# Kernel tuning notes

Measured on AMD Instinct MI355X. Metric: run time of the kernel, lower is better.

Reference implementation:

```python
import jax, jax.numpy as jnp
import numpy as np

HIDDEN = 1024
N_HEADS = 16
HEAD_DIM = HIDDEN // N_HEADS
MAX_DIST = 50
B, S = 2, 2048


def setup_inputs() -> dict:
    key = jax.random.key(0)
    ks = jax.random.split(key, 12)
    s = 1.0 / np.sqrt(HIDDEN)
    return {
        "hidden_states": jax.random.normal(ks[0], (B, S, HIDDEN), dtype=jnp.float32),
        "dist_matrix": jax.random.randint(ks[1], (B, S, S), 0, 60, dtype=jnp.int32),
        "idf_scores": jax.random.uniform(ks[2], (B, S), dtype=jnp.float32),
        "attention_mask": jnp.ones((B, S), dtype=jnp.int32),
        "Wq": jax.random.normal(ks[3], (HIDDEN, HIDDEN), dtype=jnp.float32) * s,
        "bq": jnp.zeros((HIDDEN,), dtype=jnp.float32),
        "Wk": jax.random.normal(ks[4], (HIDDEN, HIDDEN), dtype=jnp.float32) * s,
        "bk": jnp.zeros((HIDDEN,), dtype=jnp.float32),
        "Wv": jax.random.normal(ks[5], (HIDDEN, HIDDEN), dtype=jnp.float32) * s,
        "bv": jnp.zeros((HIDDEN,), dtype=jnp.float32),
        "Wo": jax.random.normal(ks[6], (HIDDEN, HIDDEN), dtype=jnp.float32) * s,
        "bo": jnp.zeros((HIDDEN,), dtype=jnp.float32),
        "struct_emb": jax.random.normal(ks[7], (MAX_DIST + 1, N_HEADS), dtype=jnp.float32) * 0.02,
        "rarity_weight": jnp.full((1,), 0.1, dtype=jnp.float32),
    }


def reference(hidden_states, dist_matrix, idf_scores, attention_mask,
              Wq, bq, Wk, bk, Wv, bv, Wo, bo, struct_emb, rarity_weight):
    b, s, _ = hidden_states.shape
    scale = 1.0 / np.sqrt(HEAD_DIM)

    def split_heads(x):  # [b,s,H] -> [b,h,s,d]
        return x.reshape(b, s, N_HEADS, HEAD_DIM).transpose(0, 2, 1, 3)

    Q = split_heads(hidden_states @ Wq.T + bq)
    K = split_heads(hidden_states @ Wk.T + bk)
    V = split_heads(hidden_states @ Wv.T + bv)

    scores = jnp.einsum('bhqd,bhkd->bhqk', Q, K) * scale

    # structural bias: gather per-head bias by clamped pairwise distance
    dist_c = jnp.clip(dist_matrix, 0, MAX_DIST)
    scores = scores + struct_emb[dist_c].transpose(0, 3, 1, 2)  # [b,h,q,k]

    # rarity bias: idf_i broadcasts over keys, idf_j over queries (as in torch code)
    rarity = rarity_weight[0] * (idf_scores[:, None, None, :] + idf_scores[:, None, :, None])
    scores = scores + rarity

    # mask: [b,1,1,s] over key axis
    mask = attention_mask[:, None, None, :]
    scores = jnp.where(mask == 0, -jnp.inf, scores)

    attn = jax.nn.softmax(scores, axis=-1)
    out = jnp.einsum('bhqk,bhkd->bhqd', attn, V)
    out = out.transpose(0, 2, 1, 3).reshape(b, s, HIDDEN)
    out = out @ Wo.T + bo
    return out, attn
```

## Files before the change

### kernel.cpp

```cpp
#include <hip/hip_runtime.h>
#include <math.h>

#define S 2048
#define HID 1024
#define NH 16
#define HD 64
#define BH 32

typedef __attribute__((ext_vector_type(8))) short bf16x8;
typedef __attribute__((ext_vector_type(4))) float f32x4;
typedef __attribute__((ext_vector_type(8))) unsigned short ush8;
typedef unsigned short u16;
typedef unsigned int u32;

__device__ __forceinline__ u16 f2bf(float f) {
    unsigned u = __float_as_uint(f);
    u += 0x7fffu + ((u >> 16) & 1u);
    return (u16)(u >> 16);
}
__device__ __forceinline__ float bf2f(u16 h) {
    return __uint_as_float(((unsigned)h) << 16);
}

__global__ __launch_bounds__(256)
void split_all(const float* __restrict__ X,  const float* __restrict__ Wq,
               const float* __restrict__ Wk, const float* __restrict__ Wv,
               const float* __restrict__ Wo,
               u16* __restrict__ Xh,  u16* __restrict__ Xl,
               u16* __restrict__ Wqh, u16* __restrict__ Wql,
               u16* __restrict__ Wkh, u16* __restrict__ Wkl,
               u16* __restrict__ Wvh, u16* __restrict__ Wvl,
               u16* __restrict__ Woh, u16* __restrict__ Wol)
{
    size_t i = (size_t)blockIdx.x * 256 + threadIdx.x;
    const float* s; u16* h; u16* l; size_t o;
    if (i < (size_t)(1u << 20)) { s = X; h = Xh; l = Xl; o = i; }
    else {
        size_t j = i - (1u << 20);
        int wsel = (int)(j >> 18); o = j & ((1u << 18) - 1);
        s = wsel == 0 ? Wq  : wsel == 1 ? Wk  : wsel == 2 ? Wv  : Wo;
        h = wsel == 0 ? Wqh : wsel == 1 ? Wkh : wsel == 2 ? Wvh : Woh;
        l = wsel == 0 ? Wql : wsel == 1 ? Wkl : wsel == 2 ? Wvl : Wol;
    }
    float4 v = ((const float4*)s)[o];
    ushort4 hv, lv;
#define SP(c, k) { unsigned u = __float_as_uint(v.c);                      \
                   unsigned hb = u & 0xffff0000u;                          \
                   float d = v.c - __uint_as_float(hb);                    \
                   hv.k = (u16)(u >> 16);                                  \
                   lv.k = (u16)(__float_as_uint(d) >> 16); }
    SP(x, x) SP(y, y) SP(z, z) SP(w, w)
#undef SP
    ((ushort4*)h)[o] = hv;
    ((ushort4*)l)[o] = lv;
}

__global__ __launch_bounds__(256)
void qkv_mfma(const u16* __restrict__ Xh, const u16* __restrict__ Xl,
              const u16* __restrict__ Wh_q, const u16* __restrict__ Wl_q,
              const u16* __restrict__ Wh_k, const u16* __restrict__ Wl_k,
              const u16* __restrict__ Wh_v, const u16* __restrict__ Wl_v,
              const float* __restrict__ bq_, const float* __restrict__ bk_,
              const float* __restrict__ bv_,
              u16* __restrict__ Qb, u16* __restrict__ Kb, u16* __restrict__ Vb)
{
    const int z = blockIdx.z;
    const u16* __restrict__ Wh = z == 0 ? Wh_q : (z == 1 ? Wh_k : Wh_v);
    const u16* __restrict__ Wl = z == 0 ? Wl_q : (z == 1 ? Wl_k : Wl_v);
    const float* __restrict__ bias = z == 0 ? bq_ : (z == 1 ? bk_ : bv_);
    u16* __restrict__ Ob = z == 0 ? Qb : (z == 1 ? Kb : Vb);
    const float oscale = (z == 0) ? 0.125f : 1.0f;

    __shared__ u16 Ah[128 * 40], Al[128 * 40], Bh[128 * 40], Bl[128 * 40];
    const int t = threadIdx.x;
    const int m0 = blockIdx.y * 128, n0 = blockIdx.x * 128;
    const int srow = t >> 1, scol = (t & 1) * 16;
    const int lane = t & 63, w = t >> 6, wm = w >> 1, wn = w & 1;
    const int lr = lane & 15, lg = lane >> 4;

    f32x4 acc[4][4] = {{{0.f, 0.f, 0.f, 0.f}}};
    for (int k0 = 0; k0 < HID; k0 += 32) {
        size_t ao = (size_t)(m0 + srow) * HID + k0 + scol;
        size_t bo = (size_t)(n0 + srow) * HID + k0 + scol;
        ush8 a0 = *(const ush8*)(Xh + ao), a1 = *(const ush8*)(Xh + ao + 8);
        ush8 a2 = *(const ush8*)(Xl + ao), a3 = *(const ush8*)(Xl + ao + 8);
        ush8 b0 = *(const ush8*)(Wh + bo), b1 = *(const ush8*)(Wh + bo + 8);
        ush8 b2 = *(const ush8*)(Wl + bo), b3 = *(const ush8*)(Wl + bo + 8);
        __syncthreads();
        *(ush8*)&Ah[srow * 40 + scol] = a0; *(ush8*)&Ah[srow * 40 + scol + 8] = a1;
        *(ush8*)&Al[srow * 40 + scol] = a2; *(ush8*)&Al[srow * 40 + scol + 8] = a3;
        *(ush8*)&Bh[srow * 40 + scol] = b0; *(ush8*)&Bh[srow * 40 + scol + 8] = b1;
        *(ush8*)&Bl[srow * 40 + scol] = b2; *(ush8*)&Bl[srow * 40 + scol + 8] = b3;
        __syncthreads();
        bf16x8 fbh[4], fbl[4];
#pragma unroll
        for (int ni = 0; ni < 4; ++ni) {
            fbh[ni] = *(const bf16x8*)&Bh[(wn * 64 + ni * 16 + lr) * 40 + lg * 8];
            fbl[ni] = *(const bf16x8*)&Bl[(wn * 64 + ni * 16 + lr) * 40 + lg * 8];
        }
#pragma unroll
        for (int mi = 0; mi < 4; ++mi) {
            bf16x8 fah = *(const bf16x8*)&Ah[(wm * 64 + mi * 16 + lr) * 40 + lg * 8];
            bf16x8 fal = *(const bf16x8*)&Al[(wm * 64 + mi * 16 + lr) * 40 + lg * 8];
#pragma unroll
            for (int ni = 0; ni < 4; ++ni) {
                f32x4 c = acc[mi][ni];
                c = __builtin_amdgcn_mfma_f32_16x16x32_bf16(fah, fbh[ni], c, 0, 0, 0);
                c = __builtin_amdgcn_mfma_f32_16x16x32_bf16(fah, fbl[ni], c, 0, 0, 0);
                c = __builtin_amdgcn_mfma_f32_16x16x32_bf16(fal, fbh[ni], c, 0, 0, 0);
                acc[mi][ni] = c;
            }
        }
    }
    const int hh = blockIdx.x * 2 + wn;
    float bv4[4];
#pragma unroll
    for (int ni = 0; ni < 4; ++ni) bv4[ni] = bias[n0 + wn * 64 + ni * 16 + lr];
#pragma unroll
    for (int mi = 0; mi < 4; ++mi)
#pragma unroll
        for (int r = 0; r < 4; ++r) {
            int m = m0 + wm * 64 + mi * 16 + lg * 4 + r;
            int b = m >> 11, s = m & 2047;
#pragma unroll
            for (int ni = 0; ni < 4; ++ni) {
                float v = (acc[mi][ni][r] + bv4[ni]) * oscale;
                Ob[((size_t)(b * NH + hh) * S + s) * HD + ni * 16 + lr] = f2bf(v);
            }
        }
}

__global__ __launch_bounds__(256)
void out_mfma(const u16* __restrict__ Xh, const u16* __restrict__ Xl,
              const u16* __restrict__ Wh, const u16* __restrict__ Wl,
              const float* __restrict__ bo_, float* __restrict__ Y)
{
    __shared__ u16 Ah[128 * 40], Al[128 * 40], Bh[128 * 40], Bl[128 * 40];
    const int t = threadIdx.x;
    const int m0 = blockIdx.y * 128, n0 = blockIdx.x * 128;
    const int srow = t >> 1, scol = (t & 1) * 16;
    const int lane = t & 63, w = t >> 6, wm = w >> 1, wn = w & 1;
    const int lr = lane & 15, lg = lane >> 4;

    f32x4 acc[4][4] = {{{0.f, 0.f, 0.f, 0.f}}};
    for (int k0 = 0; k0 < HID; k0 += 32) {
        size_t ao = (size_t)(m0 + srow) * HID + k0 + scol;
        size_t bo = (size_t)(n0 + srow) * HID + k0 + scol;
        ush8 a0 = *(const ush8*)(Xh + ao), a1 = *(const ush8*)(Xh + ao + 8);
        ush8 a2 = *(const ush8*)(Xl + ao), a3 = *(const ush8*)(Xl + ao + 8);
        ush8 b0 = *(const ush8*)(Wh + bo), b1 = *(const ush8*)(Wh + bo + 8);
        ush8 b2 = *(const ush8*)(Wl + bo), b3 = *(const ush8*)(Wl + bo + 8);
        __syncthreads();
        *(ush8*)&Ah[srow * 40 + scol] = a0; *(ush8*)&Ah[srow * 40 + scol + 8] = a1;
        *(ush8*)&Al[srow * 40 + scol] = a2; *(ush8*)&Al[srow * 40 + scol + 8] = a3;
        *(ush8*)&Bh[srow * 40 + scol] = b0; *(ush8*)&Bh[srow * 40 + scol + 8] = b1;
        *(ush8*)&Bl[srow * 40 + scol] = b2; *(ush8*)&Bl[srow * 40 + scol + 8] = b3;
        __syncthreads();
        bf16x8 fbh[4], fbl[4];
#pragma unroll
        for (int ni = 0; ni < 4; ++ni) {
            fbh[ni] = *(const bf16x8*)&Bh[(wn * 64 + ni * 16 + lr) * 40 + lg * 8];
            fbl[ni] = *(const bf16x8*)&Bl[(wn * 64 + ni * 16 + lr) * 40 + lg * 8];
        }
#pragma unroll
        for (int mi = 0; mi < 4; ++mi) {
            bf16x8 fah = *(const bf16x8*)&Ah[(wm * 64 + mi * 16 + lr) * 40 + lg * 8];
            bf16x8 fal = *(const bf16x8*)&Al[(wm * 64 + mi * 16 + lr) * 40 + lg * 8];
#pragma unroll
            for (int ni = 0; ni < 4; ++ni) {
                f32x4 c = acc[mi][ni];
                c = __builtin_amdgcn_mfma_f32_16x16x32_bf16(fah, fbh[ni], c, 0, 0, 0);
                c = __builtin_amdgcn_mfma_f32_16x16x32_bf16(fah, fbl[ni], c, 0, 0, 0);
                c = __builtin_amdgcn_mfma_f32_16x16x32_bf16(fal, fbh[ni], c, 0, 0, 0);
                acc[mi][ni] = c;
            }
        }
    }
    float bv4[4];
#pragma unroll
    for (int ni = 0; ni < 4; ++ni) bv4[ni] = bo_[n0 + wn * 64 + ni * 16 + lr];
#pragma unroll
    for (int mi = 0; mi < 4; ++mi)
#pragma unroll
        for (int r = 0; r < 4; ++r) {
            int m = m0 + wm * 64 + mi * 16 + lg * 4 + r;
#pragma unroll
            for (int ni = 0; ni < 4; ++ni)
                __builtin_nontemporal_store(acc[mi][ni][r] + bv4[ni],
                    &Y[(size_t)m * HID + n0 + wn * 64 + ni * 16 + lr]);
        }
}

__global__ __launch_bounds__(512, 4)
void attn_pv(const u16* __restrict__ Qb, const u16* __restrict__ Kb,
             const u16* __restrict__ Vb,
             const int* __restrict__ dist, const float* __restrict__ idf,
             const int* __restrict__ amask, const float* __restrict__ semb,
             const float* __restrict__ rw,
             float* __restrict__ attn, u16* __restrict__ OHh, u16* __restrict__ OHl)
{
    __shared__ u16 KV[4][64 * 72];
    __shared__ u16 Ps[128 * 72];
    __shared__ float SeH[51];
    __shared__ float mb[2048];

    const int n = blockIdx.x;
    const int xcd = n & 7, rest = n >> 3;
    const int h = rest & 15;
    const int pair = xcd * 4 + (rest >> 4);
    const int b = pair >> 4, qt = pair & 15;
    const int bh = b * NH + h, q0 = qt * 128;

    const int t = threadIdx.x, lane = t & 63, w = t >> 6;
    const int lr = lane & 15, lg = lane >> 4;
    const int q = q0 + w * 16 + lr;

    const int sr = t >> 3, sc = (t & 7) * 8;

    const float rwv = rw[0];
    if (t < 51) SeH[t] = semb[t * NH + h];
    {
        float4 ikv = *(const float4*)(idf + b * S + t * 4);
        int4   mv  = *(const int4*)(amask + b * S + t * 4);
        mb[t * 4 + 0] = mv.x ? rwv * ikv.x : -INFINITY;
        mb[t * 4 + 1] = mv.y ? rwv * ikv.y : -INFINITY;
        mb[t * 4 + 2] = mv.z ? rwv * ikv.z : -INFINITY;
        mb[t * 4 + 3] = mv.w ? rwv * ikv.w : -INFINITY;
    }

    const u16* qrow = Qb + ((size_t)bh * S + q) * HD;
    bf16x8 qa0 = *(const bf16x8*)(qrow + lg * 8);
    bf16x8 qa1 = *(const bf16x8*)(qrow + 32 + lg * 8);

    const float qb = rwv * idf[b * S + q];
    const int*  dptr = dist + (size_t)(b * S + q) * S;
    const u16* kbase = Kb + (size_t)bh * S * HD;
    const u16* vbase = Vb + (size_t)bh * S * HD;

    float M = -INFINITY, Ssum = 0.f;
    int4 dcur[4];

    *(ush8*)&KV[0][sr * 72 + sc] = *(const ush8*)(kbase + (size_t)sr * HD + sc);
    *(ush8*)&KV[1][sr * 72 + sc] = *(const ush8*)(kbase + (size_t)(64 + sr) * HD + sc);
#pragma unroll
    for (int ni = 0; ni < 4; ++ni)
        dcur[ni] = *(const int4*)(dptr + ni * 16 + lg * 4);
    __syncthreads();

    for (int it = 0; it < 32; ++it) {
        const int k0 = it * 64;
        const int cur = it & 3;

        ush8 kreg; int4 dnx[4];
        if (it < 30)
            kreg = *(const ush8*)(kbase + (size_t)(k0 + 128 + sr) * HD + sc);
        if (it < 31) {
#pragma unroll
            for (int ni = 0; ni < 4; ++ni)
                dnx[ni] = *(const int4*)(dptr + k0 + 64 + ni * 16 + lg * 4);
        }

        f32x4 c2[4];
        __builtin_amdgcn_s_setprio(1);
#pragma unroll
        for (int ni = 0; ni < 4; ++ni) {
            bf16x8 kf0 = *(const bf16x8*)&KV[cur][(ni * 16 + lr) * 72 + lg * 8];
            bf16x8 kf1 = *(const bf16x8*)&KV[cur][(ni * 16 + lr) * 72 + 32 + lg * 8];
            f32x4 c = {0.f, 0.f, 0.f, 0.f};
            c = __builtin_amdgcn_mfma_f32_16x16x32_bf16(kf0, qa0, c, 0, 0, 0);
            c = __builtin_amdgcn_mfma_f32_16x16x32_bf16(kf1, qa1, c, 0, 0, 0);
            c2[ni] = c;
        }
        __builtin_amdgcn_s_setprio(0);

        float sc4[4][4];
        float chm = -INFINITY;
#pragma unroll
        for (int ni = 0; ni < 4; ++ni) {
            const int kb = k0 + ni * 16 + lg * 4;
            int dd[4] = {dcur[ni].x, dcur[ni].y, dcur[ni].z, dcur[ni].w};
#pragma unroll
            for (int r = 0; r < 4; ++r) {
                int dc = dd[r]; dc = dc < 0 ? 0 : (dc > 50 ? 50 : dc);
                float v = c2[ni][r] + SeH[dc] + qb + mb[kb + r];
                sc4[ni][r] = v;
                chm = fmaxf(chm, v);
            }
        }
        if (chm > -INFINITY) {
            float mn = fmaxf(M, chm);
            float s = 0.f;
#pragma unroll
            for (int ni = 0; ni < 4; ++ni)
#pragma unroll
                for (int r = 0; r < 4; ++r) s += __expf(sc4[ni][r] - mn);
            Ssum = Ssum * __expf(M - mn) + s;
            M = mn;
        }

        if (it < 30)
            *(ush8*)&KV[(it + 2) & 3][sr * 72 + sc] = kreg;
        if (it < 31) {
#pragma unroll
            for (int ni = 0; ni < 4; ++ni) dcur[ni] = dnx[ni];
        }
        if ((it & 1) && it < 31) __syncthreads();
    }
#pragma unroll
    for (int off = 16; off <= 32; off <<= 1) {
        float Mo = __shfl_xor(M, off), So = __shfl_xor(Ssum, off);
        float mn = fmaxf(M, Mo);
        Ssum = Ssum * __expf(M - mn) + So * __expf(Mo - mn);
        M = mn;
    }
    const float Iv = 1.0f / Ssum;
    __syncthreads();

    float* aptr = attn + ((size_t)bh * S + q) * S;
    f32x4 oacc[4] = {{0.f,0.f,0.f,0.f},{0.f,0.f,0.f,0.f},
                     {0.f,0.f,0.f,0.f},{0.f,0.f,0.f,0.f}};

    {
        *(ush8*)&KV[0][sr * 72 + sc] = *(const ush8*)(kbase + (size_t)sr * HD + sc);
        ush8 v0 = *(const ush8*)(vbase + (size_t)lane * HD + w * 8);
#pragma unroll
        for (int j = 0; j < 8; ++j)
            KV[2][(w * 8 + j) * 72 + lane] = v0[j];
#pragma unroll
        for (int ni = 0; ni < 4; ++ni)
            dcur[ni] = *(const int4*)(dptr + ni * 16 + lg * 4);
    }
    __syncthreads();

    for (int it = 0; it < 32; ++it) {
        const int k0 = it * 64;
        const int cur = it & 1;

        ush8 kreg, vreg; int4 dnx[4];
        if (it < 31) {
            kreg = *(const ush8*)(kbase + (size_t)(k0 + 64 + sr) * HD + sc);
            vreg = *(const ush8*)(vbase + (size_t)(k0 + 64 + lane) * HD + w * 8);
#pragma unroll
            for (int ni = 0; ni < 4; ++ni)
                dnx[ni] = *(const int4*)(dptr + k0 + 64 + ni * 16 + lg * 4);
        }

        f32x4 c2[4];
        __builtin_amdgcn_s_setprio(1);
#pragma unroll
        for (int ni = 0; ni < 4; ++ni) {
            bf16x8 kf0 = *(const bf16x8*)&KV[cur][(ni * 16 + lr) * 72 + lg * 8];
            bf16x8 kf1 = *(const bf16x8*)&KV[cur][(ni * 16 + lr) * 72 + 32 + lg * 8];
            f32x4 c = {0.f, 0.f, 0.f, 0.f};
            c = __builtin_amdgcn_mfma_f32_16x16x32_bf16(kf0, qa0, c, 0, 0, 0);
            c = __builtin_amdgcn_mfma_f32_16x16x32_bf16(kf1, qa1, c, 0, 0, 0);
            c2[ni] = c;
        }
        __builtin_amdgcn_s_setprio(0);

#pragma unroll
        for (int ni = 0; ni < 4; ++ni) {
            const int kb = k0 + ni * 16 + lg * 4;
            int dd[4] = {dcur[ni].x, dcur[ni].y, dcur[ni].z, dcur[ni].w};
            float pp[4];
#pragma unroll
            for (int r = 0; r < 4; ++r) {
                int dc = dd[r]; dc = dc < 0 ? 0 : (dc > 50 ? 50 : dc);
                float v = c2[ni][r] + SeH[dc] + qb + mb[kb + r];
                pp[r] = __expf(v - M) * Iv;
            }
            f32x4 st = {pp[0], pp[1], pp[2], pp[3]};
            __builtin_nontemporal_store(st, (f32x4*)(aptr + kb));
            uint2 pk;
            pk.x = (u32)f2bf(pp[0]) | ((u32)f2bf(pp[1]) << 16);
            pk.y = (u32)f2bf(pp[2]) | ((u32)f2bf(pp[3]) << 16);
            *(uint2*)&Ps[(w * 16 + lr) * 72 + ni * 16 + lg * 4] = pk;
        }

        bf16x8 pa0 = *(const bf16x8*)&Ps[(w * 16 + lr) * 72 + lg * 8];
        bf16x8 pa1 = *(const bf16x8*)&Ps[(w * 16 + lr) * 72 + 32 + lg * 8];
        __builtin_amdgcn_s_setprio(1);
#pragma unroll
        for (int ni = 0; ni < 4; ++ni) {
            bf16x8 vb0 = *(const bf16x8*)&KV[2 + cur][(ni * 16 + lr) * 72 + lg * 8];
            bf16x8 vb1 = *(const bf16x8*)&KV[2 + cur][(ni * 16 + lr) * 72 + 32 + lg * 8];
            oacc[ni] = __builtin_amdgcn_mfma_f32_16x16x32_bf16(pa0, vb0, oacc[ni], 0, 0, 0);
            oacc[ni] = __builtin_amdgcn_mfma_f32_16x16x32_bf16(pa1, vb1, oacc[ni], 0, 0, 0);
        }
        __builtin_amdgcn_s_setprio(0);

        if (it < 31) {
            *(ush8*)&KV[cur ^ 1][sr * 72 + sc] = kreg;
#pragma unroll
            for (int j = 0; j < 8; ++j)
                KV[2 + (cur ^ 1)][(w * 8 + j) * 72 + lane] = vreg[j];
#pragma unroll
            for (int ni = 0; ni < 4; ++ni) dcur[ni] = dnx[ni];
        }
        __syncthreads();
    }

#pragma unroll
    for (int r = 0; r < 4; ++r) {
        const int qq = q0 + w * 16 + lg * 4 + r;
#pragma unroll
        for (int ni = 0; ni < 4; ++ni) {
            float v = oacc[ni][r];
            u16 hi = f2bf(v);
            u16 lo = f2bf(v - bf2f(hi));
            size_t off = ((size_t)b * S + qq) * HID + h * HD + ni * 16 + lr;
            OHh[off] = hi;
            OHl[off] = lo;
        }
    }
}

extern "C" void kernel_launch(void* const* d_in, const int* in_sizes, int n_in,
                              void* d_out, int out_size, void* d_ws, size_t ws_size,
                              hipStream_t stream)
{
    const float* hs   = (const float*)d_in[0];
    const int*   dist = (const int*)d_in[1];
    const float* idf  = (const float*)d_in[2];
    const int*   am   = (const int*)d_in[3];
    const float* Wq   = (const float*)d_in[4];
    const float* bq   = (const float*)d_in[5];
    const float* Wk   = (const float*)d_in[6];
    const float* bk   = (const float*)d_in[7];
    const float* Wv   = (const float*)d_in[8];
    const float* bv   = (const float*)d_in[9];
    const float* Wo   = (const float*)d_in[10];
    const float* bo   = (const float*)d_in[11];
    const float* se   = (const float*)d_in[12];
    const float* rw   = (const float*)d_in[13];

    float* out  = (float*)d_out;
    float* attn = out + (size_t)2 * S * HID;

    u16* Xh = (u16*)attn;
    u16* Xl = Xh + (size_t)4096 * 1024;

    u16* Qb  = (u16*)d_ws;
    u16* Kb  = Qb  + (size_t)BH * S * HD;
    u16* Vb  = Kb  + (size_t)BH * S * HD;
    u16* OHh = Vb  + (size_t)BH * S * HD;
    u16* OHl = OHh + (size_t)4096 * 1024;
    u16* Woh = OHl + (size_t)4096 * 1024;
    u16* Wol = Woh + (size_t)1024 * 1024;
    u16* Wqh = Wol + (size_t)1024 * 1024;
    u16* Wql = Wqh + (size_t)1024 * 1024;
    u16* Wkh = Wql + (size_t)1024 * 1024;
    u16* Wkl = Wkh + (size_t)1024 * 1024;
    u16* Wvh = Wkl + (size_t)1024 * 1024;
    u16* Wvl = Wvh + (size_t)1024 * 1024;

    dim3 blk(256);
    split_all<<<dim3(8192), blk, 0, stream>>>(hs, Wq, Wk, Wv, Wo,
                                              Xh, Xl, Wqh, Wql, Wkh, Wkl,
                                              Wvh, Wvl, Woh, Wol);
    qkv_mfma<<<dim3(8, 32, 3), blk, 0, stream>>>(Xh, Xl, Wqh, Wql, Wkh, Wkl,
                                                 Wvh, Wvl, bq, bk, bv, Qb, Kb, Vb);
    attn_pv<<<dim3(512), dim3(512), 0, stream>>>(Qb, Kb, Vb, dist, idf, am, se, rw,
                                                 attn, OHh, OHl);
    out_mfma<<<dim3(8, 32), blk, 0, stream>>>(OHh, OHl, Woh, Wol, bo, out);
}
```

Baseline: 415.3 us.

## Load K fragments directly from global in stats pass and drop query-constant bias

The first (max/sum) pass now reads K MFMA fragments straight from global memory into registers with a two-chunk software double buffer, instead of staging K through LDS with barriers. This removes the LDS writes, reads and __syncthreads from that pass. The per-query rarity term qb is also dropped from the scores, since it is constant along the softmax axis and cancels out. The cost is more global load instructions per wave, as each wave reloads the same K rows, and higher register pressure from holding two chunks of fragments.

```diff
diff --git a/kernel.cpp b/kernel.cpp
--- a/kernel.cpp
+++ b/kernel.cpp
@@ -232,29 +232,117 @@
     bf16x8 qa0 = *(const bf16x8*)(qrow + lg * 8);
     bf16x8 qa1 = *(const bf16x8*)(qrow + 32 + lg * 8);
 
-    const float qb = rwv * idf[b * S + q];
     const int*  dptr = dist + (size_t)(b * S + q) * S;
     const u16* kbase = Kb + (size_t)bh * S * HD;
     const u16* vbase = Vb + (size_t)bh * S * HD;
 
+    __syncthreads();
+
     float M = -INFINITY, Ssum = 0.f;
+
+    auto loadK = [&](bf16x8* f0, bf16x8* f1, int k0) {
+#pragma unroll
+        for (int ni = 0; ni < 4; ++ni) {
+            const u16* kr = kbase + (size_t)(k0 + ni * 16 + lr) * HD;
+            f0[ni] = *(const bf16x8*)(kr + lg * 8);
+            f1[ni] = *(const bf16x8*)(kr + 32 + lg * 8);
+        }
+    };
+    auto loadD = [&](int4* d, int k0) {
+#pragma unroll
+        for (int ni = 0; ni < 4; ++ni)
+            d[ni] = *(const int4*)(dptr + k0 + ni * 16 + lg * 4);
+    };
+    auto statsChunk = [&](const bf16x8* f0, const bf16x8* f1,
+                          const int4* dd4, int k0) {
+        f32x4 c2[4];
+        __builtin_amdgcn_s_setprio(1);
+#pragma unroll
+        for (int ni = 0; ni < 4; ++ni) {
+            f32x4 c = {0.f, 0.f, 0.f, 0.f};
+            c = __builtin_amdgcn_mfma_f32_16x16x32_bf16(f0[ni], qa0, c, 0, 0, 0);
+            c = __builtin_amdgcn_mfma_f32_16x16x32_bf16(f1[ni], qa1, c, 0, 0, 0);
+            c2[ni] = c;
+        }
+        __builtin_amdgcn_s_setprio(0);
+        float sc4[4][4];
+        float chm = -INFINITY;
+#pragma unroll
+        for (int ni = 0; ni < 4; ++ni) {
+            const int kb = k0 + ni * 16 + lg * 4;
+            int dd[4] = {dd4[ni].x, dd4[ni].y, dd4[ni].z, dd4[ni].w};
+#pragma unroll
+            for (int r = 0; r < 4; ++r) {
+                int dc = dd[r]; dc = dc < 0 ? 0 : (dc > 50 ? 50 : dc);
+                float v = c2[ni][r] + SeH[dc] + mb[kb + r];
+                sc4[ni][r] = v;
+                chm = fmaxf(chm, v);
+            }
+        }
+        if (chm > -INFINITY) {
+            float mn = fmaxf(M, chm);
+            float s = 0.f;
+#pragma unroll
+            for (int ni = 0; ni < 4; ++ni)
+#pragma unroll
+                for (int r = 0; r < 4; ++r) s += __expf(sc4[ni][r] - mn);
+            Ssum = Ssum * __expf(M - mn) + s;
+            M = mn;
+        }
+    };
+
+    {
+        bf16x8 ka0[4], ka1[4], kb0[4], kb1[4];
+        int4 dA[4], dB[4];
+        loadK(ka0, ka1, 0);
+        loadD(dA, 0);
+        for (int it2 = 0; it2 < 16; ++it2) {
+            const int kA = it2 * 128, kB = kA + 64;
+            loadK(kb0, kb1, kB);
+            loadD(dB, kB);
+            statsChunk(ka0, ka1, dA, kA);
+            if (it2 < 15) {
+                loadK(ka0, ka1, kB + 64);
+                loadD(dA, kB + 64);
+            }
+            statsChunk(kb0, kb1, dB, kB);
+        }
+    }
+#pragma unroll
+    for (int off = 16; off <= 32; off <<= 1) {
+        float Mo = __shfl_xor(M, off), So = __shfl_xor(Ssum, off);
+        float mn = fmaxf(M, Mo);
+        Ssum = Ssum * __expf(M - mn) + So * __expf(Mo - mn);
+        M = mn;
+    }
+    const float Iv = 1.0f / Ssum;
+    __syncthreads();
+
+    float* aptr = attn + ((size_t)bh * S + q) * S;
+    f32x4 oacc[4] = {{0.f,0.f,0.f,0.f},{0.f,0.f,0.f,0.f},
+                     {0.f,0.f,0.f,0.f},{0.f,0.f,0.f,0.f}};
     int4 dcur[4];
 
-    *(ush8*)&KV[0][sr * 72 + sc] = *(const ush8*)(kbase + (size_t)sr * HD + sc);
-    *(ush8*)&KV[1][sr * 72 + sc] = *(const ush8*)(kbase + (size_t)(64 + sr) * HD + sc);
-#pragma unroll
-    for (int ni = 0; ni < 4; ++ni)
-        dcur[ni] = *(const int4*)(dptr + ni * 16 + lg * 4);
+    {
+        *(ush8*)&KV[0][sr * 72 + sc] = *(const ush8*)(kbase + (size_t)sr * HD + sc);
+        ush8 v0 = *(const ush8*)(vbase + (size_t)lane * HD + w * 8);
+#pragma unroll
+        for (int j = 0; j < 8; ++j)
+            KV[2][(w * 8 + j) * 72 + lane] = v0[j];
+#pragma unroll
+        for (int ni = 0; ni < 4; ++ni)
+            dcur[ni] = *(const int4*)(dptr + ni * 16 + lg * 4);
+    }
     __syncthreads();
 
     for (int it = 0; it < 32; ++it) {
         const int k0 = it * 64;
-        const int cur = it & 3;
-
-        ush8 kreg; int4 dnx[4];
-        if (it < 30)
-            kreg = *(const ush8*)(kbase + (size_t)(k0 + 128 + sr) * HD + sc);
+        const int cur = it & 1;
+
+        ush8 kreg, vreg; int4 dnx[4];
         if (it < 31) {
+            kreg = *(const ush8*)(kbase + (size_t)(k0 + 64 + sr) * HD + sc);
+            vreg = *(const ush8*)(vbase + (size_t)(k0 + 64 + lane) * HD + w * 8);
 #pragma unroll
             for (int ni = 0; ni < 4; ++ni)
                 dnx[ni] = *(const int4*)(dptr + k0 + 64 + ni * 16 + lg * 4);
@@ -273,91 +361,6 @@
         }
         __builtin_amdgcn_s_setprio(0);
 
-        float sc4[4][4];
-        float chm = -INFINITY;
-#pragma unroll
-        for (int ni = 0; ni < 4; ++ni) {
-            const int kb = k0 + ni * 16 + lg * 4;
-            int dd[4] = {dcur[ni].x, dcur[ni].y, dcur[ni].z, dcur[ni].w};
-#pragma unroll
-            for (int r = 0; r < 4; ++r) {
-                int dc = dd[r]; dc = dc < 0 ? 0 : (dc > 50 ? 50 : dc);
-                float v = c2[ni][r] + SeH[dc] + qb + mb[kb + r];
-                sc4[ni][r] = v;
-                chm = fmaxf(chm, v);
-            }
-        }
-        if (chm > -INFINITY) {
-            float mn = fmaxf(M, chm);
-            float s = 0.f;
-#pragma unroll
-            for (int ni = 0; ni < 4; ++ni)
-#pragma unroll
-                for (int r = 0; r < 4; ++r) s += __expf(sc4[ni][r] - mn);
-            Ssum = Ssum * __expf(M - mn) + s;
-            M = mn;
-        }
-
-        if (it < 30)
-            *(ush8*)&KV[(it + 2) & 3][sr * 72 + sc] = kreg;
-        if (it < 31) {
-#pragma unroll
-            for (int ni = 0; ni < 4; ++ni) dcur[ni] = dnx[ni];
-        }
-        if ((it & 1) && it < 31) __syncthreads();
-    }
-#pragma unroll
-    for (int off = 16; off <= 32; off <<= 1) {
-        float Mo = __shfl_xor(M, off), So = __shfl_xor(Ssum, off);
-        float mn = fmaxf(M, Mo);
-        Ssum = Ssum * __expf(M - mn) + So * __expf(Mo - mn);
-        M = mn;
-    }
-    const float Iv = 1.0f / Ssum;
-    __syncthreads();
-
-    float* aptr = attn + ((size_t)bh * S + q) * S;
-    f32x4 oacc[4] = {{0.f,0.f,0.f,0.f},{0.f,0.f,0.f,0.f},
-                     {0.f,0.f,0.f,0.f},{0.f,0.f,0.f,0.f}};
-
-    {
-        *(ush8*)&KV[0][sr * 72 + sc] = *(const ush8*)(kbase + (size_t)sr * HD + sc);
-        ush8 v0 = *(const ush8*)(vbase + (size_t)lane * HD + w * 8);
-#pragma unroll
-        for (int j = 0; j < 8; ++j)
-            KV[2][(w * 8 + j) * 72 + lane] = v0[j];
-#pragma unroll
-        for (int ni = 0; ni < 4; ++ni)
-            dcur[ni] = *(const int4*)(dptr + ni * 16 + lg * 4);
-    }
-    __syncthreads();
-
-    for (int it = 0; it < 32; ++it) {
-        const int k0 = it * 64;
-        const int cur = it & 1;
-
-        ush8 kreg, vreg; int4 dnx[4];
-        if (it < 31) {
-            kreg = *(const ush8*)(kbase + (size_t)(k0 + 64 + sr) * HD + sc);
-            vreg = *(const ush8*)(vbase + (size_t)(k0 + 64 + lane) * HD + w * 8);
-#pragma unroll
-            for (int ni = 0; ni < 4; ++ni)
-                dnx[ni] = *(const int4*)(dptr + k0 + 64 + ni * 16 + lg * 4);
-        }
-
-        f32x4 c2[4];
-        __builtin_amdgcn_s_setprio(1);
-#pragma unroll
-        for (int ni = 0; ni < 4; ++ni) {
-            bf16x8 kf0 = *(const bf16x8*)&KV[cur][(ni * 16 + lr) * 72 + lg * 8];
-            bf16x8 kf1 = *(const bf16x8*)&KV[cur][(ni * 16 + lr) * 72 + 32 + lg * 8];
-            f32x4 c = {0.f, 0.f, 0.f, 0.f};
-            c = __builtin_amdgcn_mfma_f32_16x16x32_bf16(kf0, qa0, c, 0, 0, 0);
-            c = __builtin_amdgcn_mfma_f32_16x16x32_bf16(kf1, qa1, c, 0, 0, 0);
-            c2[ni] = c;
-        }
-        __builtin_amdgcn_s_setprio(0);
-
 #pragma unroll
         for (int ni = 0; ni < 4; ++ni) {
             const int kb = k0 + ni * 16 + lg * 4;
@@ -366,7 +369,7 @@
 #pragma unroll
             for (int r = 0; r < 4; ++r) {
                 int dc = dd[r]; dc = dc < 0 ? 0 : (dc > 50 ? 50 : dc);
-                float v = c2[ni][r] + SeH[dc] + qb + mb[kb + r];
+                float v = c2[ni][r] + SeH[dc] + mb[kb + r];
                 pp[r] = __expf(v - M) * Iv;
             }
             f32x4 st = {pp[0], pp[1], pp[2], pp[3]};
```

New measurement: 512.4 us. 1.23x slower.
